# Kernel tuning notes

Measured on AMD Instinct MI355X. Metric: run time of the kernel, lower is better.

Reference implementation:

```python
import jax, jax.numpy as jnp
import numpy as np

B, T, S, D = 8, 64, 256, 512


def setup_inputs() -> dict:
    key = jax.random.key(0)
    ks = jax.random.split(key, 8)
    scale = 1.0 / np.sqrt(D)
    return {
        "source": jax.random.normal(ks[0], (B, T, D), jnp.float32),
        "memory_bank": jax.random.normal(ks[1], (B, S, D), jnp.float32),
        "source_masks": jnp.ones((B, T), jnp.float32),
        # params (torch Linear stored as [out,in]; here as [in,out] so y = x @ W + b)
        "Wq": jax.random.normal(ks[2], (D, D), jnp.float32) * scale,
        "bq": jnp.zeros((D,), jnp.float32),
        "Wv": jax.random.normal(ks[3], (D, D), jnp.float32) * scale,
        "Wc": jax.random.normal(ks[4], (2 * D, 2), jnp.float32) * scale,
        "bc": jnp.zeros((2,), jnp.float32),
    }


def reference(source, memory_bank, source_masks, Wq, bq, Wv, Wc, bc):
    # accumulate(): running mean over segments == cumsum / (1..T), then mask
    counts = jnp.arange(1, T + 1, dtype=source.dtype)  # [T]
    acc = jnp.cumsum(source, axis=1) / counts[None, :, None]  # [B,T,D]
    acc = acc * source_masks[:, :, None]

    # score(): h_t = linear_query(acc); gate = v(tanh(h_t + h_s)) broadcast over (t,s)
    ht = acc @ Wq + bq  # [B,T,D]
    gate = jnp.tanh(ht[:, :, None, :] + memory_bank[:, None, :, :]) @ Wv  # [B,T,S,D]
    sum_gate = gate.sum(axis=-1)  # [B,T,S]

    # linear_cate(cat([h_s, sum_gate*h_s], -1)) split as two [D,2] matmuls;
    # sum_gate is a per-(b,t,s) scalar so (sum_gate*h_s)@Wc2 == sum_gate*(h_s@Wc2).
    part1 = memory_bank @ Wc[:D]  # [B,S,2]
    part2 = memory_bank @ Wc[D:]  # [B,S,2]
    h_fuse = part1[:, None] + sum_gate[..., None] * part2[:, None] + bc  # [B,T,S,2]
    return h_fuse
```

## Files before the change

### kernel.cpp

```cpp
#include <hip/hip_runtime.h>

constexpr int B = 8, T = 64, S = 256, D = 512;
constexpr float SCL = 2.885390081777927f;

__global__ __launch_bounds__(128) void k1_acc(const float* __restrict__ src,
                                              const float* __restrict__ mask,
                                              float* __restrict__ acc) {
    int blk = blockIdx.x;
    int b = blk >> 4, tc = (blk >> 2) & 3, dc = blk & 3;
    int d = dc * 128 + threadIdx.x;
    const float* sp = src + ((size_t)b * T) * D + d;
    const float* mp = mask + b * T;
    float* ap = acc + ((size_t)b * T) * D + d;
    float run = 0.f;
    for (int ch = 0; ch <= tc; ++ch) {
        float v[16];
#pragma unroll
        for (int i = 0; i < 16; ++i) v[i] = sp[(size_t)(ch * 16 + i) * D];
        if (ch < tc) {
#pragma unroll
            for (int i = 0; i < 16; ++i) run += v[i];
        } else {
#pragma unroll
            for (int i = 0; i < 16; ++i) {
                run += v[i];
                int t = ch * 16 + i;
                ap[(size_t)t * D] = run * __builtin_amdgcn_rcpf((float)(t + 1)) * mp[t];
            }
        }
    }
}

__global__ __launch_bounds__(128) void k2_htwp(const float* __restrict__ acc,
                                               const float* __restrict__ Wq,
                                               const float* __restrict__ bq,
                                               const float* __restrict__ Wv,
                                               const float* __restrict__ mem,
                                               const float* __restrict__ Wc,
                                               const float* __restrict__ bc,
                                               float* __restrict__ ht,
                                               float* __restrict__ wv,
                                               float* __restrict__ part1,
                                               float* __restrict__ part2) {
    const int blk = blockIdx.x;
    const int tid = threadIdx.x;
    if (blk < 256) {
        __shared__ float AL[32][34];
        __shared__ float BL[32][36];
        const int r0 = (blk >> 4) * 32;
        const int c0 = (blk & 15) * 32;
        const int tx = tid & 7, ty = tid >> 3;
        float s00 = 0, s01 = 0, s02 = 0, s03 = 0, s10 = 0, s11 = 0, s12 = 0, s13 = 0;
        for (int d0 = 0; d0 < D; d0 += 32) {
            __syncthreads();
#pragma unroll
            for (int k = 0; k < 2; ++k) {
                int idx = tid + k * 128;
                int row = idx >> 3;
                int c4 = (idx & 7) * 4;
                float4 va = *(const float4*)(acc + (size_t)(r0 + row) * D + d0 + c4);
                AL[c4 + 0][row] = va.x; AL[c4 + 1][row] = va.y;
                AL[c4 + 2][row] = va.z; AL[c4 + 3][row] = va.w;
                float4 vb = *(const float4*)(Wq + (size_t)(d0 + row) * D + c0 + c4);
                *(float4*)&BL[row][c4] = vb;
            }
            __syncthreads();
#pragma unroll
            for (int dd = 0; dd < 32; ++dd) {
                float2 a = *(const float2*)&AL[dd][ty * 2];
                float4 bv = *(const float4*)&BL[dd][tx * 4];
                s00 = fmaf(a.x, bv.x, s00); s01 = fmaf(a.x, bv.y, s01);
                s02 = fmaf(a.x, bv.z, s02); s03 = fmaf(a.x, bv.w, s03);
                s10 = fmaf(a.y, bv.x, s10); s11 = fmaf(a.y, bv.y, s11);
                s12 = fmaf(a.y, bv.z, s12); s13 = fmaf(a.y, bv.w, s13);
            }
        }
        int r = r0 + ty * 2, c = c0 + tx * 4;
        float4 bqv = *(const float4*)(bq + c);
        *(float4*)(ht + (size_t)r * D + c) = make_float4(
            (s00 + bqv.x) * SCL, (s01 + bqv.y) * SCL, (s02 + bqv.z) * SCL, (s03 + bqv.w) * SCL);
        *(float4*)(ht + (size_t)(r + 1) * D + c) = make_float4(
            (s10 + bqv.x) * SCL, (s11 + bqv.y) * SCL, (s12 + bqv.z) * SCL, (s13 + bqv.w) * SCL);
    } else if (blk < 288) {
        int w = tid >> 6, lane = tid & 63;
        int base = (blk - 256) * 16 + w * 8;
        for (int it = 0; it < 8; ++it) {
            int row = base + it;
            const float* r = Wv + (size_t)row * D;
            float s = 0.f;
#pragma unroll
            for (int j = 0; j < D / 64; ++j) s += r[lane + j * 64];
#pragma unroll
            for (int off = 32; off; off >>= 1) s += __shfl_down(s, off);
            if (lane == 0) wv[row] = s;
        }
    } else {
        int w = tid >> 6, lane = tid & 63;
        int base = (blk - 288) * 16 + w * 8;
        for (int it = 0; it < 8; ++it) {
            int row = base + it;
            const float* mrow = mem + (size_t)row * D;
            float a0 = 0, a1 = 0, a2 = 0, a3 = 0;
#pragma unroll
            for (int j = 0; j < D / 64; ++j) {
                int d = lane + j * 64;
                float m = mrow[d];
                float2 w1 = *(const float2*)(Wc + d * 2);
                float2 w2 = *(const float2*)(Wc + (D + d) * 2);
                a0 = fmaf(m, w1.x, a0); a1 = fmaf(m, w1.y, a1);
                a2 = fmaf(m, w2.x, a2); a3 = fmaf(m, w2.y, a3);
            }
#pragma unroll
            for (int off = 32; off; off >>= 1) {
                a0 += __shfl_down(a0, off);
                a1 += __shfl_down(a1, off);
                a2 += __shfl_down(a2, off);
                a3 += __shfl_down(a3, off);
            }
            if (lane == 0) {
                part1[row * 2 + 0] = a0 + bc[0];
                part1[row * 2 + 1] = a1 + bc[1];
                part2[row * 2 + 0] = a2;
                part2[row * 2 + 1] = a3;
            }
        }
    }
}

__global__ __launch_bounds__(256) void k3_gate(const float* __restrict__ ht,
                                               const float* __restrict__ mem,
                                               const float* __restrict__ wv,
                                               const float* __restrict__ part1,
                                               const float* __restrict__ part2,
                                               float* __restrict__ out) {
    __shared__ float htT[64][18];
    __shared__ float memT[64][36];
    __shared__ float wvL[64];
    __shared__ float pt[4][16][33];
    const int tid = threadIdx.x;
    const int sb = blockIdx.x, tb = blockIdx.y, b = blockIdx.z;
    const int lane = tid & 63, w = tid >> 6;
    const int ss = lane & 7, tt = lane >> 3;
    const float* htBase = ht + ((size_t)b * T + tb * 16) * D;
    const float* memBase = mem + ((size_t)b * S + sb * 32) * D;
    const int hrow = tid >> 4;
    const int c4 = (tid & 15) * 4;
    const int mrow1 = hrow + 16;
    float4 ph = *(const float4*)(htBase + (size_t)hrow * D + c4);
    float4 pm0 = *(const float4*)(memBase + (size_t)hrow * D + c4);
    float4 pm1 = *(const float4*)(memBase + (size_t)mrow1 * D + c4);
    float4 pw;
    if (tid < 16) pw = *(const float4*)(wv + tid * 4);
    float a[2][4];
#pragma unroll
    for (int r = 0; r < 2; ++r)
#pragma unroll
        for (int j = 0; j < 4; ++j) a[r][j] = 0.f;
#pragma unroll 1
    for (int c = 0; c < 8; ++c) {
        __syncthreads();
        htT[c4 + 0][hrow] = ph.x; htT[c4 + 1][hrow] = ph.y;
        htT[c4 + 2][hrow] = ph.z; htT[c4 + 3][hrow] = ph.w;
        memT[c4 + 0][hrow] = pm0.x * SCL; memT[c4 + 1][hrow] = pm0.y * SCL;
        memT[c4 + 2][hrow] = pm0.z * SCL; memT[c4 + 3][hrow] = pm0.w * SCL;
        memT[c4 + 0][mrow1] = pm1.x * SCL; memT[c4 + 1][mrow1] = pm1.y * SCL;
        memT[c4 + 2][mrow1] = pm1.z * SCL; memT[c4 + 3][mrow1] = pm1.w * SCL;
        if (tid < 16) {
            wvL[tid * 4 + 0] = pw.x; wvL[tid * 4 + 1] = pw.y;
            wvL[tid * 4 + 2] = pw.z; wvL[tid * 4 + 3] = pw.w;
        }
        __syncthreads();
        if (c < 7) {
            int d0 = (c + 1) * 64;
            ph = *(const float4*)(htBase + (size_t)hrow * D + d0 + c4);
            pm0 = *(const float4*)(memBase + (size_t)hrow * D + d0 + c4);
            pm1 = *(const float4*)(memBase + (size_t)mrow1 * D + d0 + c4);
            if (tid < 16) pw = *(const float4*)(wv + d0 + tid * 4);
        }
        const int dbase = w * 16;
#pragma unroll
        for (int i = 0; i < 16; ++i) {
            int dd = dbase + i;
            float2 h2 = *(const float2*)&htT[dd][tt * 2];
            float4 m4 = *(const float4*)&memT[dd][ss * 4];
            float wvv = wvL[dd];
            float hs[2] = {h2.x, h2.y};
            float ms[4] = {m4.x, m4.y, m4.z, m4.w};
#pragma unroll
            for (int r = 0; r < 2; ++r)
#pragma unroll
                for (int j = 0; j < 4; ++j) {
                    float e = __builtin_amdgcn_exp2f(hs[r] + ms[j]);
                    float th = fmaf(-2.0f, __builtin_amdgcn_rcpf(e + 1.0f), 1.0f);
                    a[r][j] = fmaf(wvv, th, a[r][j]);
                }
        }
    }
    __syncthreads();
#pragma unroll
    for (int r = 0; r < 2; ++r)
#pragma unroll
        for (int j = 0; j < 4; ++j) pt[w][tt * 2 + r][ss * 4 + j] = a[r][j];
    __syncthreads();
    const int t = tid >> 4;
    const int s0 = (tid & 15) * 2;
    float sg0 = pt[0][t][s0] + pt[1][t][s0] + pt[2][t][s0] + pt[3][t][s0];
    float sg1 = pt[0][t][s0 + 1] + pt[1][t][s0 + 1] + pt[2][t][s0 + 1] + pt[3][t][s0 + 1];
    const int srow = b * S + sb * 32 + s0;
    float4 p1 = *(const float4*)(part1 + (size_t)srow * 2);
    float4 p2 = *(const float4*)(part2 + (size_t)srow * 2);
    float* o = out + (((size_t)b * T + tb * 16 + t) * S + sb * 32 + s0) * 2;
    *(float4*)o = make_float4(p1.x + sg0 * p2.x, p1.y + sg0 * p2.y,
                              p1.z + sg1 * p2.z, p1.w + sg1 * p2.w);
}

extern "C" void kernel_launch(void* const* d_in, const int* in_sizes, int n_in,
                              void* d_out, int out_size, void* d_ws, size_t ws_size,
                              hipStream_t stream) {
    const float* source = (const float*)d_in[0];
    const float* memory = (const float*)d_in[1];
    const float* masks  = (const float*)d_in[2];
    const float* Wq = (const float*)d_in[3];
    const float* bq = (const float*)d_in[4];
    const float* Wv = (const float*)d_in[5];
    const float* Wc = (const float*)d_in[6];
    const float* bc = (const float*)d_in[7];
    float* out = (float*)d_out;
    float* ws = (float*)d_ws;

    float* accp  = ws;
    float* ht    = accp + B * T * D;
    float* wv    = ht + B * T * D;
    float* part1 = wv + D;
    float* part2 = part1 + B * S * 2;

    k1_acc<<<128, 128, 0, stream>>>(source, masks, accp);
    k2_htwp<<<416, 128, 0, stream>>>(accp, Wq, bq, Wv, memory, Wc, bc,
                                     ht, wv, part1, part2);
    k3_gate<<<dim3(8, 4, 8), 256, 0, stream>>>(ht, memory, wv, part1, part2, out);
}
```

Measured before the change: 111.8 us.

## Use bf16 MFMA for query projection and simplify tanh accumulation

The fp32 FMA tiled GEMM for acc@Wq is replaced with a bf16 MFMA kernel that loads whole 32x512 panels into swizzled LDS via global_load_lds. The prep kernel now also writes acc in bf16 and a transposed bf16 copy of Wq. The Wq transpose is recomputed on every call. In the gate kernel, tanh = 1 - 2/(e+1) is rewritten so the inner loop only accumulates wv/(e+1), and the constant sum of wv is applied once at the end. Together these cut per-element ALU work and the GEMM cost, at the price of bf16 precision in the projection.

```diff
diff --git a/kernel.cpp b/kernel.cpp
--- a/kernel.cpp
+++ b/kernel.cpp
@@ -1,89 +1,79 @@
 #include <hip/hip_runtime.h>
+#include <hip/hip_bf16.h>
 
 constexpr int B = 8, T = 64, S = 256, D = 512;
 constexpr float SCL = 2.885390081777927f;
 
-__global__ __launch_bounds__(128) void k1_acc(const float* __restrict__ src,
-                                              const float* __restrict__ mask,
-                                              float* __restrict__ acc) {
-    int blk = blockIdx.x;
-    int b = blk >> 4, tc = (blk >> 2) & 3, dc = blk & 3;
-    int d = dc * 128 + threadIdx.x;
-    const float* sp = src + ((size_t)b * T) * D + d;
-    const float* mp = mask + b * T;
-    float* ap = acc + ((size_t)b * T) * D + d;
-    float run = 0.f;
-    for (int ch = 0; ch <= tc; ++ch) {
-        float v[16];
-#pragma unroll
-        for (int i = 0; i < 16; ++i) v[i] = sp[(size_t)(ch * 16 + i) * D];
-        if (ch < tc) {
-#pragma unroll
-            for (int i = 0; i < 16; ++i) run += v[i];
-        } else {
-#pragma unroll
-            for (int i = 0; i < 16; ++i) {
-                run += v[i];
-                int t = ch * 16 + i;
-                ap[(size_t)t * D] = run * __builtin_amdgcn_rcpf((float)(t + 1)) * mp[t];
-            }
-        }
-    }
-}
-
-__global__ __launch_bounds__(128) void k2_htwp(const float* __restrict__ acc,
+typedef __attribute__((ext_vector_type(8))) short bf16x8;
+typedef __attribute__((ext_vector_type(4))) float f32x4;
+
+__device__ __forceinline__ unsigned short f2b(float f) {
+    __hip_bfloat16 h = __float2bfloat16(f);
+    return __builtin_bit_cast(unsigned short, h);
+}
+
+__global__ __launch_bounds__(128) void k1_prep(const float* __restrict__ src,
+                                               const float* __restrict__ mask,
                                                const float* __restrict__ Wq,
-                                               const float* __restrict__ bq,
                                                const float* __restrict__ Wv,
                                                const float* __restrict__ mem,
                                                const float* __restrict__ Wc,
                                                const float* __restrict__ bc,
-                                               float* __restrict__ ht,
+                                               __hip_bfloat16* __restrict__ accB,
+                                               __hip_bfloat16* __restrict__ WqTB,
                                                float* __restrict__ wv,
                                                float* __restrict__ part1,
                                                float* __restrict__ part2) {
+    __shared__ float TS[64][66];
     const int blk = blockIdx.x;
     const int tid = threadIdx.x;
-    if (blk < 256) {
-        __shared__ float AL[32][34];
-        __shared__ float BL[32][36];
-        const int r0 = (blk >> 4) * 32;
-        const int c0 = (blk & 15) * 32;
-        const int tx = tid & 7, ty = tid >> 3;
-        float s00 = 0, s01 = 0, s02 = 0, s03 = 0, s10 = 0, s11 = 0, s12 = 0, s13 = 0;
-        for (int d0 = 0; d0 < D; d0 += 32) {
-            __syncthreads();
-#pragma unroll
-            for (int k = 0; k < 2; ++k) {
-                int idx = tid + k * 128;
-                int row = idx >> 3;
-                int c4 = (idx & 7) * 4;
-                float4 va = *(const float4*)(acc + (size_t)(r0 + row) * D + d0 + c4);
-                AL[c4 + 0][row] = va.x; AL[c4 + 1][row] = va.y;
-                AL[c4 + 2][row] = va.z; AL[c4 + 3][row] = va.w;
-                float4 vb = *(const float4*)(Wq + (size_t)(d0 + row) * D + c0 + c4);
-                *(float4*)&BL[row][c4] = vb;
-            }
-            __syncthreads();
-#pragma unroll
-            for (int dd = 0; dd < 32; ++dd) {
-                float2 a = *(const float2*)&AL[dd][ty * 2];
-                float4 bv = *(const float4*)&BL[dd][tx * 4];
-                s00 = fmaf(a.x, bv.x, s00); s01 = fmaf(a.x, bv.y, s01);
-                s02 = fmaf(a.x, bv.z, s02); s03 = fmaf(a.x, bv.w, s03);
-                s10 = fmaf(a.y, bv.x, s10); s11 = fmaf(a.y, bv.y, s11);
-                s12 = fmaf(a.y, bv.z, s12); s13 = fmaf(a.y, bv.w, s13);
-            }
-        }
-        int r = r0 + ty * 2, c = c0 + tx * 4;
-        float4 bqv = *(const float4*)(bq + c);
-        *(float4*)(ht + (size_t)r * D + c) = make_float4(
-            (s00 + bqv.x) * SCL, (s01 + bqv.y) * SCL, (s02 + bqv.z) * SCL, (s03 + bqv.w) * SCL);
-        *(float4*)(ht + (size_t)(r + 1) * D + c) = make_float4(
-            (s10 + bqv.x) * SCL, (s11 + bqv.y) * SCL, (s12 + bqv.z) * SCL, (s13 + bqv.w) * SCL);
-    } else if (blk < 288) {
+    if (blk < 128) {
+        int b = blk >> 4, tc = (blk >> 2) & 3, dc = blk & 3;
+        int d = dc * 128 + tid;
+        const float* sp = src + ((size_t)b * T) * D + d;
+        const float* mp = mask + b * T;
+        __hip_bfloat16* ap = accB + ((size_t)b * T) * D + d;
+        float run = 0.f;
+        for (int ch = 0; ch <= tc; ++ch) {
+            float v[16];
+#pragma unroll
+            for (int i = 0; i < 16; ++i) v[i] = sp[(size_t)(ch * 16 + i) * D];
+            if (ch < tc) {
+#pragma unroll
+                for (int i = 0; i < 16; ++i) run += v[i];
+            } else {
+#pragma unroll
+                for (int i = 0; i < 16; ++i) {
+                    run += v[i];
+                    int t = ch * 16 + i;
+                    float val = run * __builtin_amdgcn_rcpf((float)(t + 1)) * mp[t];
+                    ap[(size_t)t * D] = __float2bfloat16(val);
+                }
+            }
+        }
+    } else if (blk < 192) {
+        int tb = blk - 128;
+        int r0 = (tb >> 3) * 64, c0 = (tb & 7) * 64;
+        int r = tid >> 1, h = tid & 1;
+#pragma unroll
+        for (int j = 0; j < 8; ++j) {
+            int col = h * 32 + j * 4;
+            float4 v = *(const float4*)(Wq + (size_t)(r0 + r) * D + c0 + col);
+            *(float4*)&TS[r][col] = v;
+        }
+        __syncthreads();
+        int n = tid >> 1;
+#pragma unroll
+        for (int j = 0; j < 8; ++j) {
+            int kk = h * 32 + j * 4;
+            ushort4 u;
+            u.x = f2b(TS[kk + 0][n]); u.y = f2b(TS[kk + 1][n]);
+            u.z = f2b(TS[kk + 2][n]); u.w = f2b(TS[kk + 3][n]);
+            *(ushort4*)((unsigned short*)WqTB + (size_t)(c0 + n) * D + r0 + kk) = u;
+        }
+    } else if (blk < 224) {
         int w = tid >> 6, lane = tid & 63;
-        int base = (blk - 256) * 16 + w * 8;
+        int base = (blk - 192) * 16 + w * 8;
         for (int it = 0; it < 8; ++it) {
             int row = base + it;
             const float* r = Wv + (size_t)row * D;
@@ -96,7 +86,7 @@
         }
     } else {
         int w = tid >> 6, lane = tid & 63;
-        int base = (blk - 288) * 16 + w * 8;
+        int base = (blk - 224) * 16 + w * 8;
         for (int it = 0; it < 8; ++it) {
             int row = base + it;
             const float* mrow = mem + (size_t)row * D;
@@ -124,6 +114,58 @@
                 part2[row * 2 + 1] = a3;
             }
         }
+    }
+}
+
+__global__ __launch_bounds__(64) void k2_gemm(const __hip_bfloat16* __restrict__ accB,
+                                              const __hip_bfloat16* __restrict__ WqTB,
+                                              const float* __restrict__ bq,
+                                              float* __restrict__ ht) {
+    __shared__ unsigned short Asw[32 * 512];
+    __shared__ unsigned short Bsw[32 * 512];
+    const int tid = threadIdx.x;
+    const int r0 = (blockIdx.x >> 4) * 32;
+    const int c0 = (blockIdx.x & 15) * 32;
+    const unsigned short* Ag = (const unsigned short*)accB;
+    const unsigned short* Bg = (const unsigned short*)WqTB;
+#pragma unroll
+    for (int j = 0; j < 32; ++j) {
+        int chunk = tid ^ (j & 7);
+        __builtin_amdgcn_global_load_lds(
+            (const __attribute__((address_space(1))) unsigned int*)(Ag + (size_t)(r0 + j) * D + chunk * 8),
+            (__attribute__((address_space(3))) unsigned int*)&Asw[j * 512], 16, 0, 0);
+        __builtin_amdgcn_global_load_lds(
+            (const __attribute__((address_space(1))) unsigned int*)(Bg + (size_t)(c0 + j) * D + chunk * 8),
+            (__attribute__((address_space(3))) unsigned int*)&Bsw[j * 512], 16, 0, 0);
+    }
+    asm volatile("s_waitcnt vmcnt(0)" ::: "memory");
+    const int lr = tid & 15;
+    const int g = tid >> 4;
+    f32x4 acc00 = {0,0,0,0}, acc01 = {0,0,0,0}, acc10 = {0,0,0,0}, acc11 = {0,0,0,0};
+    const char* Ab = (const char*)Asw;
+    const char* Bb = (const char*)Bsw;
+#pragma unroll
+    for (int ks = 0; ks < 16; ++ks) {
+        int kc = ks * 4 + g;
+        int ra0 = lr, ra1 = 16 + lr;
+        bf16x8 a0 = *(const bf16x8*)(Ab + ra0 * 1024 + ((kc ^ (ra0 & 7)) * 16));
+        bf16x8 a1 = *(const bf16x8*)(Ab + ra1 * 1024 + ((kc ^ (ra1 & 7)) * 16));
+        bf16x8 b0 = *(const bf16x8*)(Bb + ra0 * 1024 + ((kc ^ (ra0 & 7)) * 16));
+        bf16x8 b1 = *(const bf16x8*)(Bb + ra1 * 1024 + ((kc ^ (ra1 & 7)) * 16));
+        acc00 = __builtin_amdgcn_mfma_f32_16x16x32_bf16(a0, b0, acc00, 0, 0, 0);
+        acc01 = __builtin_amdgcn_mfma_f32_16x16x32_bf16(a0, b1, acc01, 0, 0, 0);
+        acc10 = __builtin_amdgcn_mfma_f32_16x16x32_bf16(a1, b0, acc10, 0, 0, 0);
+        acc11 = __builtin_amdgcn_mfma_f32_16x16x32_bf16(a1, b1, acc11, 0, 0, 0);
+    }
+    const int col0 = c0 + lr, col1 = c0 + 16 + lr;
+    const int rb = r0 + g * 4;
+    float bq0 = bq[col0], bq1 = bq[col1];
+#pragma unroll
+    for (int r = 0; r < 4; ++r) {
+        ht[(size_t)(rb + r) * D + col0]      = (acc00[r] + bq0) * SCL;
+        ht[(size_t)(rb + r) * D + col1]      = (acc01[r] + bq1) * SCL;
+        ht[(size_t)(rb + 16 + r) * D + col0] = (acc10[r] + bq0) * SCL;
+        ht[(size_t)(rb + 16 + r) * D + col1] = (acc11[r] + bq1) * SCL;
     }
 }
 
@@ -137,6 +179,7 @@
     __shared__ float memT[64][36];
     __shared__ float wvL[64];
     __shared__ float pt[4][16][33];
+    __shared__ float wsL[4];
     const int tid = threadIdx.x;
     const int sb = blockIdx.x, tb = blockIdx.y, b = blockIdx.z;
     const int lane = tid & 63, w = tid >> 6;
@@ -156,6 +199,7 @@
     for (int r = 0; r < 2; ++r)
 #pragma unroll
         for (int j = 0; j < 4; ++j) a[r][j] = 0.f;
+    float wsum = 0.f;
 #pragma unroll 1
     for (int c = 0; c < 8; ++c) {
         __syncthreads();
@@ -184,6 +228,7 @@
             float2 h2 = *(const float2*)&htT[dd][tt * 2];
             float4 m4 = *(const float4*)&memT[dd][ss * 4];
             float wvv = wvL[dd];
+            wsum += wvv;
             float hs[2] = {h2.x, h2.y};
             float ms[4] = {m4.x, m4.y, m4.z, m4.w};
 #pragma unroll
@@ -191,8 +236,7 @@
 #pragma unroll
                 for (int j = 0; j < 4; ++j) {
                     float e = __builtin_amdgcn_exp2f(hs[r] + ms[j]);
-                    float th = fmaf(-2.0f, __builtin_amdgcn_rcpf(e + 1.0f), 1.0f);
-                    a[r][j] = fmaf(wvv, th, a[r][j]);
+                    a[r][j] = fmaf(wvv, __builtin_amdgcn_rcpf(e + 1.0f), a[r][j]);
                 }
         }
     }
@@ -201,11 +245,15 @@
     for (int r = 0; r < 2; ++r)
 #pragma unroll
         for (int j = 0; j < 4; ++j) pt[w][tt * 2 + r][ss * 4 + j] = a[r][j];
+    if (lane == 0) wsL[w] = wsum;
     __syncthreads();
     const int t = tid >> 4;
     const int s0 = (tid & 15) * 2;
-    float sg0 = pt[0][t][s0] + pt[1][t][s0] + pt[2][t][s0] + pt[3][t][s0];
-    float sg1 = pt[0][t][s0 + 1] + pt[1][t][s0 + 1] + pt[2][t][s0 + 1] + pt[3][t][s0 + 1];
+    float Wsum = wsL[0] + wsL[1] + wsL[2] + wsL[3];
+    float q0 = pt[0][t][s0] + pt[1][t][s0] + pt[2][t][s0] + pt[3][t][s0];
+    float q1 = pt[0][t][s0 + 1] + pt[1][t][s0 + 1] + pt[2][t][s0 + 1] + pt[3][t][s0 + 1];
+    float sg0 = fmaf(-2.0f, q0, Wsum);
+    float sg1 = fmaf(-2.0f, q1, Wsum);
     const int srow = b * S + sb * 32 + s0;
     float4 p1 = *(const float4*)(part1 + (size_t)srow * 2);
     float4 p2 = *(const float4*)(part2 + (size_t)srow * 2);
@@ -226,16 +274,17 @@
     const float* Wc = (const float*)d_in[6];
     const float* bc = (const float*)d_in[7];
     float* out = (float*)d_out;
-    float* ws = (float*)d_ws;
-
-    float* accp  = ws;
-    float* ht    = accp + B * T * D;
-    float* wv    = ht + B * T * D;
+    char* w = (char*)d_ws;
+
+    __hip_bfloat16* accB = (__hip_bfloat16*)w;
+    __hip_bfloat16* WqTB = (__hip_bfloat16*)(w + (512 << 10));
+    float* ht    = (float*)(w + (1024 << 10));
+    float* wv    = (float*)(w + (2048 << 10));
     float* part1 = wv + D;
     float* part2 = part1 + B * S * 2;
 
-    k1_acc<<<128, 128, 0, stream>>>(source, masks, accp);
-    k2_htwp<<<416, 128, 0, stream>>>(accp, Wq, bq, Wv, memory, Wc, bc,
-                                     ht, wv, part1, part2);
+    k1_prep<<<352, 128, 0, stream>>>(source, masks, Wq, Wv, memory, Wc, bc,
+                                     accB, WqTB, wv, part1, part2);
+    k2_gemm<<<256, 64, 0, stream>>>(accB, WqTB, bq, ht);
     k3_gate<<<dim3(8, 4, 8), 256, 0, stream>>>(ht, memory, wv, part1, part2, out);
 }
```

New measurement: 100.6 us. 1.11x faster.
